# Kernel tuning notes

Hardware: AMD Instinct MI355X
Metric: run time of the kernel (lower is better)

The kernel has to match this reference:

```python
import jax, jax.numpy as jnp
import numpy as np

H = W = 128          # image shape
N_RGC = 32           # grid side -> 1024 RGCs per polarity
L = 1.0
K_POS = 0.155
V1_DIM = 64          # -> 4096 V1 units


def _build_model():
    rng = np.random.default_rng(0)
    pos = np.array([[i, j] for i in range(-N_RGC // 2, N_RGC // 2)
                    for j in range(-N_RGC // 2, N_RGC // 2)], dtype=np.float64)
    M = L * np.array([[1.0, 1.0], [np.sqrt(3.0), -np.sqrt(3.0)]])
    on_locs = pos @ M.T + rng.normal(0.0, K_POS * L, size=pos.shape)
    off_locs = pos @ M.T + rng.normal(0.0, K_POS * L, size=pos.shape)
    half = L * (N_RGC // 2)
    # clip (instead of filter) so RGC count is deterministic; boundary-only effect
    on_locs = np.clip(on_locs, -half, half)
    off_locs = np.clip(off_locs, -half, half)
    scale = H / (2.0 * half)
    on_locs = (on_locs + half) * scale
    off_locs = (off_locs + half) * scale
    locs = np.concatenate([on_locs, off_locs])          # [2048, 2]
    signs = np.concatenate([np.ones(len(on_locs)), -np.ones(len(off_locs))])
    sigma = 0.7 * L * scale

    # vectorized Gaussian RGC kernels: act[n, r, c] = exp(-((c-x_n)^2+(r-y_n)^2)/(2 sigma^2))
    gx = np.arange(H)[None, :] - locs[:, 0:1]           # [N, H] (column offsets)
    gy = np.arange(W)[None, :] - locs[:, 1:2]           # [N, W] (row offsets)
    acts = np.exp(-(gx[:, None, :] ** 2 + gy[:, :, None] ** 2) / (2.0 * sigma ** 2))
    acts = np.where(acts < 1e-5, 0.0, acts)
    acts /= acts.sum(axis=(1, 2), keepdims=True)
    acts *= signs[:, None, None]                        # [2048, 128, 128]

    n_rgc = locs.shape[0]
    lgn_idx = rng.integers(0, n_rgc, size=int(n_rgc * 1.5))  # [3072]
    lgn_locs = np.concatenate([locs, locs[lgn_idx]])         # [5120, 2]

    # V1 retinotopic grid
    X, Y = np.meshgrid(np.linspace(0, H, num=V1_DIM, endpoint=True),
                       np.linspace(0, W, num=V1_DIM, endpoint=True))
    v1_locs = np.vstack([X.ravel(), Y.ravel()]).T            # [4096, 2]

    # LGN->V1 connectivity (dense materialization of the CSR matrix)
    d2 = ((v1_locs[:, None, :] - lgn_locs[None, :, :]) ** 2).sum(-1)  # [4096, 5120]
    radius = 200.0 * sigma
    within = d2 <= radius ** 2
    p = (rng.random(d2.shape) >= 0.85 * np.exp(-d2 / (2.0 * sigma * 0.97))).astype(np.float64)
    conn = np.where(within, p * np.exp(-d2 / (2.0 * sigma * 1.1)), 0.0)

    return (acts[:n_rgc // 2].astype(np.float32),
            acts[n_rgc // 2:].astype(np.float32),
            conn.astype(np.float32),
            lgn_idx.astype(np.int32))


def setup_inputs() -> dict:
    key = jax.random.key(0)
    act_on, act_off, conn, lgn_idx = _build_model()
    x = jax.random.uniform(key, (H, W), dtype=jnp.float32)
    return {"x": x,
            "act_on": jnp.asarray(act_on),
            "act_off": jnp.asarray(act_off),
            "conn": jnp.asarray(conn),
            "lgn_idx": jnp.asarray(lgn_idx)}


def reference(x, act_on, act_off, conn, lgn_idx):
    # RGC stage: elementwise modulation of Gaussian kernels by image / inverted image
    n = act_on.shape[0] + act_off.shape[0]
    r = jnp.concatenate([x[None, :, :] * act_on,
                         (1.0 - x)[None, :, :] * act_off], axis=0).reshape(n, -1)  # [2048, 16384]
    # LGN stage: gather-based duplication
    l = jnp.concatenate([r, r[lgn_idx]], axis=0)                                    # [5120, 16384]
    # V1 stage: connectivity matmul (original: CSR SpMM)
    v = conn @ l                                                                    # [4096, 16384]
    return (r, l, v)
```

## Files before the change

kernel.cpp:

```cpp
#include <hip/hip_runtime.h>
#include <hip/hip_bf16.h>

#define NPIX   16384
#define NRROWS 2048
#define NLROWS 5120
#define NVROWS 4096
#define GK     5120
#define KF     2048
#define KEXTRA 3072
#define BK8    64
#define KTILES (KF / BK8)
#define NCB    (NPIX / 256)
#define TAU    1e-4f

using f32x4    = __attribute__((ext_vector_type(4))) float;
using bf16x8   = __attribute__((ext_vector_type(8))) __bf16;
using ushortx8 = __attribute__((ext_vector_type(8))) unsigned short;

__device__ __forceinline__ unsigned short f2b(float f) {
    union { float f; unsigned u; } v; v.f = f;
    unsigned r = (v.u + 0x7FFFu + ((v.u >> 16) & 1u)) >> 16;
    return (unsigned short)r;
}

#define GLOAD_LDS16(gsrc, ldst)                                                        \
    __builtin_amdgcn_global_load_lds(                                                  \
        (const __attribute__((address_space(1))) void*)(gsrc),                         \
        (__attribute__((address_space(3))) void*)(ldst), 16, 0, 0)

__global__ __launch_bounds__(256) void prep_kernel(const int* __restrict__ lgn_idx,
                                                   int* __restrict__ order,
                                                   int* __restrict__ inv_off,
                                                   int* __restrict__ inv_j,
                                                   unsigned int* __restrict__ amask) {
    __shared__ int bins[64];
    __shared__ int cnt[KF];
    __shared__ int part[256];
    __shared__ int spart[257];
    const int t = threadIdx.x;
    if (t < 64) bins[t] = 0;
    if (t < 16) amask[t] = 0u;
    __syncthreads();
    for (int k = t; k < KF; k += 256) {
        int base = k & 1023;
        int key = ((base >> 5) - (base & 31)) + 31;
        atomicAdd(&bins[key], 1);
    }
    __syncthreads();
    if (t == 0) {
        int run = 0;
        for (int b = 0; b < 63; ++b) { int c = bins[b]; bins[b] = run; run += c; }
    }
    __syncthreads();
    for (int k = t; k < KF; k += 256) {
        int base = k & 1023;
        int key = ((base >> 5) - (base & 31)) + 31;
        int slot = atomicAdd(&bins[key], 1);
        order[slot] = k;
    }
    for (int i = t; i < KF; i += 256) cnt[i] = 0;
    __syncthreads();
    for (int j = t; j < KEXTRA; j += 256) atomicAdd(&cnt[lgn_idx[j]], 1);
    __syncthreads();
    const int base8 = t * 8;
    int local[8];
    {
        int s = 0;
        #pragma unroll
        for (int i = 0; i < 8; ++i) { local[i] = s; s += cnt[base8 + i]; }
        part[t] = s;
    }
    __syncthreads();
    if (t == 0) {
        int run = 0;
        for (int i = 0; i < 256; ++i) { spart[i] = run; run += part[i]; }
        spart[256] = run;
    }
    __syncthreads();
    #pragma unroll
    for (int i = 0; i < 8; ++i) {
        int o = spart[t] + local[i];
        inv_off[base8 + i] = o;
        cnt[base8 + i] = o;
    }
    if (t == 0) inv_off[KF] = spart[256];
    __syncthreads();
    for (int j = t; j < KEXTRA; j += 256) {
        int s = atomicAdd(&cnt[lgn_idx[j]], 1);
        inv_j[s] = j;
    }
}

__global__ __launch_bounds__(256) void combo_kernel(const float* __restrict__ x,
                                                    const float* __restrict__ act_on,
                                                    const float* __restrict__ act_off,
                                                    const float* __restrict__ conn,
                                                    const int* __restrict__ lgn_idx,
                                                    const int* __restrict__ order,
                                                    const int* __restrict__ inv_off,
                                                    const int* __restrict__ inv_j,
                                                    float* __restrict__ r,
                                                    float* __restrict__ l,
                                                    unsigned short* __restrict__ rbt,
                                                    unsigned char* __restrict__ nzb,
                                                    unsigned short* __restrict__ Ab,
                                                    unsigned int* __restrict__ amask) {
    __shared__ unsigned short tile[64][66];
    __shared__ float acc[KF];
    __shared__ int nzf;
    __shared__ unsigned int rmask;
    const int t = threadIdx.x;

    if (blockIdx.y < KTILES) {
        const int k0 = blockIdx.y * 64;
        const int n0 = blockIdx.x * 64;
        if (t == 0) nzf = 0;
        __syncthreads();
        #pragma unroll
        for (int p = 0; p < 4; ++p) {
            int row  = p * 16 + (t >> 4);
            int kk   = k0 + row;
            int lrow = order[kk];
            int c4   = t & 15;
            int px   = n0 + c4 * 4;
            float4 xv = *reinterpret_cast<const float4*>(&x[px]);
            float4 d;
            if (lrow < 1024) {
                float4 a = *reinterpret_cast<const float4*>(&act_on[(size_t)lrow * NPIX + px]);
                d.x = xv.x * a.x; d.y = xv.y * a.y; d.z = xv.z * a.z; d.w = xv.w * a.w;
            } else {
                float4 a = *reinterpret_cast<const float4*>(&act_off[(size_t)(lrow - 1024) * NPIX + px]);
                d.x = (1.f - xv.x) * a.x; d.y = (1.f - xv.y) * a.y;
                d.z = (1.f - xv.z) * a.z; d.w = (1.f - xv.w) * a.w;
            }
            *reinterpret_cast<float4*>(&l[(size_t)lrow * NPIX + px]) = d;
            *reinterpret_cast<float4*>(&r[(size_t)lrow * NPIX + px]) = d;
            int e0 = inv_off[lrow], e1 = inv_off[lrow + 1];
            for (int e = e0; e < e1; ++e)
                *reinterpret_cast<float4*>(&l[(size_t)(NRROWS + inv_j[e]) * NPIX + px]) = d;
            tile[row][c4 * 4 + 0] = f2b(d.x);
            tile[row][c4 * 4 + 1] = f2b(d.y);
            tile[row][c4 * 4 + 2] = f2b(d.z);
            tile[row][c4 * 4 + 3] = f2b(d.w);
            if (d.x != 0.f || d.y != 0.f || d.z != 0.f || d.w != 0.f) nzf = 1;
        }
        __syncthreads();
        #pragma unroll
        for (int p = 0; p < 4; ++p) {
            int nn = p * 16 + (t >> 4);
            int k4 = t & 15;
            ushort4 s;
            s.x = tile[k4 * 4 + 0][nn];
            s.y = tile[k4 * 4 + 1][nn];
            s.z = tile[k4 * 4 + 2][nn];
            s.w = tile[k4 * 4 + 3][nn];
            *reinterpret_cast<ushort4*>(&rbt[(size_t)(n0 + nn) * KF + k0 + k4 * 4]) = s;
        }
        if (t == 0) nzb[blockIdx.y * 256 + blockIdx.x] = (unsigned char)nzf;
    } else {
        const int row = (blockIdx.y - KTILES) * 256 + blockIdx.x;
        if (t == 0) rmask = 0u;
        const float* crow = conn + (size_t)row * GK;
        #pragma unroll
        for (int i = 0; i < KF / 256; ++i)
            acc[t + 256 * i] = crow[t + 256 * i];
        __syncthreads();
        #pragma unroll
        for (int j = 0; j < KEXTRA / 256; ++j) {
            int jj = t + 256 * j;
            float v = crow[KF + jj];
            atomicAdd(&acc[lgn_idx[jj]], v);
        }
        __syncthreads();
        unsigned int local = 0u;
        #pragma unroll
        for (int i = 0; i < KF / 256; ++i) {
            int c = t + 256 * i;
            float v = acc[order[c]];
            Ab[(size_t)row * KF + c] = f2b(v);
            if (fabsf(v) >= TAU) local |= 1u << (c >> 6);
        }
        atomicOr(&rmask, local);
        __syncthreads();
        if (t == 0) atomicOr(&amask[row >> 8], rmask);
    }
}

__global__ __launch_bounds__(64) void bmask_build_kernel(const unsigned char* __restrict__ nzb,
                                                         unsigned int* __restrict__ bmask) {
    const int c = threadIdx.x;
    unsigned int m = 0u;
    for (int kt = 0; kt < KTILES; ++kt) {
        const unsigned char* p = nzb + kt * 256 + c * 4;
        if (p[0] | p[1] | p[2] | p[3]) m |= 1u << kt;
    }
    bmask[c] = m;
}

__global__ __launch_bounds__(512, 2) void gemm8_kernel(const unsigned short* __restrict__ Ab,
                                                       const unsigned short* __restrict__ Bb,
                                                       const unsigned int* __restrict__ bmask,
                                                       const unsigned int* __restrict__ amask,
                                                       float* __restrict__ C) {
    __shared__ unsigned short lds[2][2][256][64];
    __shared__ int s_klist[KTILES];
    __shared__ int s_cnt;

    const int tid  = threadIdx.x;
    const int lane = tid & 63;
    const int wid  = tid >> 6;
    const int wm   = wid >> 2;
    const int wn   = wid & 3;

    int bid = blockIdx.x;
    int swz = (bid & 7) * 128 + (bid >> 3);
    int mb  = swz & 15;
    int nb  = swz >> 4;
    const int row0 = mb * 256;
    const int col0 = nb * 256;

    if (tid == 0) {
        unsigned int m = bmask[nb] & amask[mb];
        int c = 0;
        while (m) { int kt = __ffs(m) - 1; m &= m - 1u; s_klist[c++] = kt; }
        s_cnt = c;
    }
    __syncthreads();
    const int cnt = s_cnt;

    const int strow = tid >> 3;
    const int gc    = (lane & 7) ^ (lane >> 3);

#define STAGE_A(buf, rnd, kt)                                                          \
    GLOAD_LDS16(&Ab[(size_t)(row0 + (rnd) * 64 + strow) * KF + (kt) * BK8 + gc * 8],   \
                &lds[buf][0][(rnd) * 64 + strow][(lane & 7) * 8])
#define STAGE_B(buf, rnd, kt)                                                          \
    GLOAD_LDS16(&Bb[(size_t)(col0 + (rnd) * 64 + strow) * KF + (kt) * BK8 + gc * 8],   \
                &lds[buf][1][(rnd) * 64 + strow][(lane & 7) * 8])
#define FRAG(buf, op, row, c)                                                          \
    __builtin_bit_cast(bf16x8, *reinterpret_cast<const ushortx8*>(                     \
        &lds[buf][op][row][(((c) ^ ((row) & 7)) * 8)]))

    f32x4 acc[2][2][4][2] = {};
    const int fr = lane & 15;
    const int kg = lane >> 4;

    bf16x8 af[2][4][2];
    bf16x8 b[2][2];

    if (cnt > 0) {
        const int kt0 = s_klist[0];
        STAGE_A(0, 0, kt0); STAGE_A(0, 1, kt0); STAGE_A(0, 2, kt0); STAGE_A(0, 3, kt0);
        STAGE_B(0, 0, kt0); STAGE_B(0, 1, kt0); STAGE_B(0, 2, kt0); STAGE_B(0, 3, kt0);
        asm volatile("s_waitcnt vmcnt(2)" ::: "memory");
        __builtin_amdgcn_s_barrier();

        for (int t = 0; t < cnt - 1; ++t) {
            const int cur = t & 1;
            const int nxt = cur ^ 1;
            const int ktn = s_klist[t + 1];

            #pragma unroll
            for (int m = 0; m < 4; ++m)
                #pragma unroll
                for (int ks = 0; ks < 2; ++ks)
                    af[0][m][ks] = FRAG(cur, 0, wm * 64 + m * 16 + fr, ks * 4 + kg);
            #pragma unroll
            for (int n = 0; n < 2; ++n)
                #pragma unroll
                for (int ks = 0; ks < 2; ++ks)
                    b[n][ks] = FRAG(cur, 1, wn * 32 + n * 16 + fr, ks * 4 + kg);
            STAGE_A(nxt, 0, ktn); STAGE_A(nxt, 1, ktn);
            STAGE_A(nxt, 2, ktn); STAGE_A(nxt, 3, ktn);
            __builtin_amdgcn_s_setprio(1);
            #pragma unroll
            for (int m = 0; m < 4; ++m)
                #pragma unroll
                for (int n = 0; n < 2; ++n)
                    #pragma unroll
                    for (int ks = 0; ks < 2; ++ks)
                        acc[0][0][m][n] = __builtin_amdgcn_mfma_f32_16x16x32_bf16(af[0][m][ks], b[n][ks], acc[0][0][m][n], 0, 0, 0);
            __builtin_amdgcn_s_setprio(0);

            #pragma unroll
            for (int m = 0; m < 4; ++m)
                #pragma unroll
                for (int ks = 0; ks < 2; ++ks)
                    af[1][m][ks] = FRAG(cur, 0, 128 + wm * 64 + m * 16 + fr, ks * 4 + kg);
            STAGE_B(nxt, 0, ktn); STAGE_B(nxt, 1, ktn);
            STAGE_B(nxt, 2, ktn); STAGE_B(nxt, 3, ktn);
            __builtin_amdgcn_s_setprio(1);
            #pragma unroll
            for (int m = 0; m < 4; ++m)
                #pragma unroll
                for (int n = 0; n < 2; ++n)
                    #pragma unroll
                    for (int ks = 0; ks < 2; ++ks)
                        acc[1][0][m][n] = __builtin_amdgcn_mfma_f32_16x16x32_bf16(af[1][m][ks], b[n][ks], acc[1][0][m][n], 0, 0, 0);
            __builtin_amdgcn_s_setprio(0);
            asm volatile("s_waitcnt vmcnt(8)" ::: "memory");
            __builtin_amdgcn_s_barrier();

            #pragma unroll
            for (int n = 0; n < 2; ++n)
                #pragma unroll
                for (int ks = 0; ks < 2; ++ks)
                    b[n][ks] = FRAG(cur, 1, 128 + wn * 32 + n * 16 + fr, ks * 4 + kg);
            __builtin_amdgcn_s_setprio(1);
            #pragma unroll
            for (int m = 0; m < 4; ++m)
                #pragma unroll
                for (int n = 0; n < 2; ++n)
                    #pragma unroll
                    for (int ks = 0; ks < 2; ++ks)
                        acc[1][1][m][n] = __builtin_amdgcn_mfma_f32_16x16x32_bf16(af[1][m][ks], b[n][ks], acc[1][1][m][n], 0, 0, 0);
            __builtin_amdgcn_s_setprio(0);

            __builtin_amdgcn_s_setprio(1);
            #pragma unroll
            for (int m = 0; m < 4; ++m)
                #pragma unroll
                for (int n = 0; n < 2; ++n)
                    #pragma unroll
                    for (int ks = 0; ks < 2; ++ks)
                        acc[0][1][m][n] = __builtin_amdgcn_mfma_f32_16x16x32_bf16(af[0][m][ks], b[n][ks], acc[0][1][m][n], 0, 0, 0);
            __builtin_amdgcn_s_setprio(0);
            asm volatile("s_waitcnt vmcnt(2)" ::: "memory");
            __builtin_amdgcn_s_barrier();
        }

        {
            const int cur = (cnt - 1) & 1;
            #pragma unroll
            for (int m = 0; m < 4; ++m)
                #pragma unroll
                for (int ks = 0; ks < 2; ++ks) {
                    af[0][m][ks] = FRAG(cur, 0, wm * 64 + m * 16 + fr, ks * 4 + kg);
                    af[1][m][ks] = FRAG(cur, 0, 128 + wm * 64 + m * 16 + fr, ks * 4 + kg);
                }
            #pragma unroll
            for (int n = 0; n < 2; ++n)
                #pragma unroll
                for (int ks = 0; ks < 2; ++ks)
                    b[n][ks] = FRAG(cur, 1, wn * 32 + n * 16 + fr, ks * 4 + kg);
            #pragma unroll
            for (int m = 0; m < 4; ++m)
                #pragma unroll
                for (int n = 0; n < 2; ++n)
                    #pragma unroll
                    for (int ks = 0; ks < 2; ++ks) {
                        acc[0][0][m][n] = __builtin_amdgcn_mfma_f32_16x16x32_bf16(af[0][m][ks], b[n][ks], acc[0][0][m][n], 0, 0, 0);
                        acc[1][0][m][n] = __builtin_amdgcn_mfma_f32_16x16x32_bf16(af[1][m][ks], b[n][ks], acc[1][0][m][n], 0, 0, 0);
                    }
            asm volatile("s_waitcnt vmcnt(0)" ::: "memory");
            __builtin_amdgcn_s_barrier();
            #pragma unroll
            for (int n = 0; n < 2; ++n)
                #pragma unroll
                for (int ks = 0; ks < 2; ++ks)
                    b[n][ks] = FRAG(cur, 1, 128 + wn * 32 + n * 16 + fr, ks * 4 + kg);
            #pragma unroll
            for (int m = 0; m < 4; ++m)
                #pragma unroll
                for (int n = 0; n < 2; ++n)
                    #pragma unroll
                    for (int ks = 0; ks < 2; ++ks) {
                        acc[1][1][m][n] = __builtin_amdgcn_mfma_f32_16x16x32_bf16(af[1][m][ks], b[n][ks], acc[1][1][m][n], 0, 0, 0);
                        acc[0][1][m][n] = __builtin_amdgcn_mfma_f32_16x16x32_bf16(af[0][m][ks], b[n][ks], acc[0][1][m][n], 0, 0, 0);
                    }
        }
    }

    #pragma unroll
    for (int qm = 0; qm < 2; ++qm)
        #pragma unroll
        for (int qn = 0; qn < 2; ++qn)
            #pragma unroll
            for (int m = 0; m < 4; ++m)
                #pragma unroll
                for (int n = 0; n < 2; ++n) {
                    int rr = row0 + qm * 128 + wm * 64 + m * 16 + kg * 4;
                    int cc = col0 + qn * 128 + wn * 32 + n * 16 + fr;
                    #pragma unroll
                    for (int j = 0; j < 4; ++j)
                        C[(size_t)(rr + j) * NPIX + cc] = acc[qm][qn][m][n][j];
                }
#undef STAGE_A
#undef STAGE_B
#undef FRAG
}

__global__ __launch_bounds__(256) void rgc_kernel(const float* __restrict__ x,
                                                  const float* __restrict__ act_on,
                                                  const float* __restrict__ act_off,
                                                  float* __restrict__ r) {
    unsigned f = blockIdx.x * 256u + threadIdx.x;
    unsigned n  = f >> 12;
    unsigned p4 = f & 4095u;
    float4 xv = reinterpret_cast<const float4*>(x)[p4];
    float4 a, o;
    if (n < 1024u) {
        a = reinterpret_cast<const float4*>(act_on)[(size_t)n * 4096u + p4];
        o.x = xv.x * a.x; o.y = xv.y * a.y; o.z = xv.z * a.z; o.w = xv.w * a.w;
    } else {
        a = reinterpret_cast<const float4*>(act_off)[(size_t)(n - 1024u) * 4096u + p4];
        o.x = (1.f - xv.x) * a.x; o.y = (1.f - xv.y) * a.y;
        o.z = (1.f - xv.z) * a.z; o.w = (1.f - xv.w) * a.w;
    }
    reinterpret_cast<float4*>(r)[f] = o;
}

__global__ __launch_bounds__(256) void lgn_kernel(const float* __restrict__ r,
                                                  const int* __restrict__ lgn_idx,
                                                  float* __restrict__ l) {
    unsigned f = blockIdx.x * 256u + threadIdx.x;
    unsigned k  = f >> 12;
    unsigned p4 = f & 4095u;
    unsigned src = (k < 2048u) ? k : (unsigned)lgn_idx[k - 2048u];
    reinterpret_cast<float4*>(l)[f] =
        reinterpret_cast<const float4*>(r)[(size_t)src * 4096u + p4];
}

__global__ __launch_bounds__(256) void gemm_fallback_kernel(const float* __restrict__ A,
                                                            const float* __restrict__ B,
                                                            float* __restrict__ C) {
    const int tid  = threadIdx.x;
    const int lane = tid & 63;
    const int wid  = tid >> 6;
    const int wr   = wid >> 1;
    const int wc   = wid & 1;
    const int row0 = blockIdx.y * 128;
    const int col0 = blockIdx.x * 128;

    __shared__ unsigned short As[4][128][8];
    __shared__ unsigned short Bs[4][128][8];

    f32x4 acc[4][4] = {};

    for (int k0 = 0; k0 < GK; k0 += 32) {
        #pragma unroll
        for (int i = 0; i < 4; ++i) {
            int f  = tid + 256 * i;
            int rr = f >> 3;
            int c4 = f & 7;
            float4 d = *reinterpret_cast<const float4*>(
                &A[(size_t)(row0 + rr) * GK + k0 + c4 * 4]);
            ushort4 s;
            s.x = f2b(d.x); s.y = f2b(d.y); s.z = f2b(d.z); s.w = f2b(d.w);
            *reinterpret_cast<ushort4*>(&As[c4 >> 1][rr][(c4 & 1) * 4]) = s;
        }
        #pragma unroll
        for (int i = 0; i < 4; ++i) {
            int f  = tid + 256 * i;
            int kk = f >> 5;
            int c4 = f & 31;
            float4 d = *reinterpret_cast<const float4*>(
                &B[(size_t)(k0 + kk) * NPIX + col0 + c4 * 4]);
            int g = kk >> 3, j = kk & 7;
            Bs[g][c4 * 4 + 0][j] = f2b(d.x);
            Bs[g][c4 * 4 + 1][j] = f2b(d.y);
            Bs[g][c4 * 4 + 2][j] = f2b(d.z);
            Bs[g][c4 * 4 + 3][j] = f2b(d.w);
        }
        __syncthreads();

        const int fr = lane & 15;
        const int kg = lane >> 4;
        bf16x8 af[4], bfr[4];
        #pragma unroll
        for (int m = 0; m < 4; ++m)
            af[m] = __builtin_bit_cast(bf16x8,
                *reinterpret_cast<const ushortx8*>(&As[kg][wr * 64 + m * 16 + fr][0]));
        #pragma unroll
        for (int n = 0; n < 4; ++n)
            bfr[n] = __builtin_bit_cast(bf16x8,
                *reinterpret_cast<const ushortx8*>(&Bs[kg][wc * 64 + n * 16 + fr][0]));
        #pragma unroll
        for (int m = 0; m < 4; ++m)
            #pragma unroll
            for (int n = 0; n < 4; ++n)
                acc[m][n] = __builtin_amdgcn_mfma_f32_16x16x32_bf16(af[m], bfr[n], acc[m][n], 0, 0, 0);
        __syncthreads();
    }

    #pragma unroll
    for (int m = 0; m < 4; ++m) {
        #pragma unroll
        for (int n = 0; n < 4; ++n) {
            int rr = row0 + wr * 64 + m * 16 + ((lane >> 4) << 2);
            int cc = col0 + wc * 64 + n * 16 + (lane & 15);
            #pragma unroll
            for (int j = 0; j < 4; ++j)
                C[(size_t)(rr + j) * NPIX + cc] = acc[m][n][j];
        }
    }
}

extern "C" void kernel_launch(void* const* d_in, const int* in_sizes, int n_in,
                              void* d_out, int out_size, void* d_ws, size_t ws_size,
                              hipStream_t stream) {
    const float* x       = (const float*)d_in[0];
    const float* act_on  = (const float*)d_in[1];
    const float* act_off = (const float*)d_in[2];
    const float* conn    = (const float*)d_in[3];
    const int*   lgn_idx = (const int*)d_in[4];

    float* out = (float*)d_out;
    float* r = out;
    float* l = out + (size_t)NRROWS * NPIX;
    float* v = out + (size_t)(NRROWS + NLROWS) * NPIX;

    const size_t rbt_bytes  = (size_t)NPIX * KF * sizeof(unsigned short);
    const size_t conn_bytes = (size_t)NVROWS * KF * sizeof(unsigned short);
    const size_t small_bytes = (KF + (KF + 1) + KEXTRA + NCB + 16 + 64) * sizeof(int)
                             + KTILES * 256;

    if (ws_size >= rbt_bytes + conn_bytes + small_bytes) {
        char* wsp = (char*)d_ws;
        unsigned short* rbt    = (unsigned short*)wsp;                wsp += rbt_bytes;
        unsigned short* connb  = (unsigned short*)wsp;                wsp += conn_bytes;
        int*            order  = (int*)wsp;                           wsp += KF * sizeof(int);
        int*            invoff = (int*)wsp;                           wsp += (KF + 1) * sizeof(int);
        int*            invj   = (int*)wsp;                           wsp += KEXTRA * sizeof(int);
        unsigned char*  nzb    = (unsigned char*)wsp;                 wsp += KTILES * 256;
        unsigned int*   bmask  = (unsigned int*)wsp;                  wsp += NCB * sizeof(int);
        unsigned int*   amask  = (unsigned int*)wsp;

        prep_kernel<<<1, 256, 0, stream>>>(lgn_idx, order, invoff, invj, amask);
        dim3 tg(NPIX / 64, KTILES + NVROWS / 256);
        combo_kernel<<<tg, 256, 0, stream>>>(x, act_on, act_off, conn, lgn_idx, order,
                                             invoff, invj, r, l, rbt, nzb, connb, amask);
        bmask_build_kernel<<<1, 64, 0, stream>>>(nzb, bmask);
        gemm8_kernel<<<(NVROWS / 256) * (NPIX / 256), 512, 0, stream>>>(connb, rbt, bmask, amask, v);
    } else {
        rgc_kernel<<<(NRROWS * (NPIX / 4)) / 256, 256, 0, stream>>>(x, act_on, act_off, r);
        lgn_kernel<<<(NLROWS * (NPIX / 4)) / 256, 256, 0, stream>>>(r, lgn_idx, l);
        dim3 grid(NPIX / 128, NVROWS / 128);
        gemm_fallback_kernel<<<grid, 256, 0, stream>>>(conn, l, v);
    }
}
```

Measured before the change: 313.2 us.

## Halve GEMM K-step to 32, raise occupancy, fold block-mask build into GEMM

Shrinks the LDS staging tile from 64 to 32 K elements, which halves shared memory per block and fragment registers, and raises launch bounds from 2 to 4 blocks per CU. The separate bmask_build kernel is removed: each GEMM block reads its nonzero flags from nzb directly and expands every active 64-wide tile into two 32-wide K steps. The aim is more latency hiding from higher occupancy and one fewer kernel launch. In exchange there are twice as many barriers and loop iterations per tile, and the LDS XOR swizzle is dropped, which may bring back bank conflicts.

After: 619.3 us. +97.7%, slower.

```diff
diff --git a/kernel.cpp b/kernel.cpp
--- a/kernel.cpp
+++ b/kernel.cpp
@@ -8,8 +8,7 @@
 #define GK     5120
 #define KF     2048
 #define KEXTRA 3072
-#define BK8    64
-#define KTILES (KF / BK8)
+#define KTILES 32
 #define NCB    (NPIX / 256)
 #define TAU    1e-4f
 
@@ -186,24 +185,14 @@
     }
 }
 
-__global__ __launch_bounds__(64) void bmask_build_kernel(const unsigned char* __restrict__ nzb,
-                                                         unsigned int* __restrict__ bmask) {
-    const int c = threadIdx.x;
-    unsigned int m = 0u;
-    for (int kt = 0; kt < KTILES; ++kt) {
-        const unsigned char* p = nzb + kt * 256 + c * 4;
-        if (p[0] | p[1] | p[2] | p[3]) m |= 1u << kt;
-    }
-    bmask[c] = m;
-}
-
-__global__ __launch_bounds__(512, 2) void gemm8_kernel(const unsigned short* __restrict__ Ab,
+__global__ __launch_bounds__(512, 4) void gemm8_kernel(const unsigned short* __restrict__ Ab,
                                                        const unsigned short* __restrict__ Bb,
-                                                       const unsigned int* __restrict__ bmask,
+                                                       const unsigned char* __restrict__ nzb,
                                                        const unsigned int* __restrict__ amask,
                                                        float* __restrict__ C) {
-    __shared__ unsigned short lds[2][2][256][64];
-    __shared__ int s_klist[KTILES];
+    __shared__ unsigned short lds[2][2][256][32];
+    __shared__ unsigned int s_ok[KTILES];
+    __shared__ int s_klist[2 * KTILES];
     __shared__ int s_cnt;
 
     const int tid  = threadIdx.x;
@@ -219,101 +208,89 @@
     const int row0 = mb * 256;
     const int col0 = nb * 256;
 
+    if (tid < KTILES)
+        s_ok[tid] = reinterpret_cast<const unsigned int*>(nzb)[tid * 64 + nb];
+    __syncthreads();
     if (tid == 0) {
-        unsigned int m = bmask[nb] & amask[mb];
+        unsigned int am = amask[mb];
         int c = 0;
-        while (m) { int kt = __ffs(m) - 1; m &= m - 1u; s_klist[c++] = kt; }
+        for (int kt = 0; kt < KTILES; ++kt)
+            if (s_ok[kt] && ((am >> kt) & 1u)) { s_klist[c++] = kt * 2; s_klist[c++] = kt * 2 + 1; }
         s_cnt = c;
     }
     __syncthreads();
     const int cnt = s_cnt;
 
-    const int strow = tid >> 3;
-    const int gc    = (lane & 7) ^ (lane >> 3);
-
-#define STAGE_A(buf, rnd, kt)                                                          \
-    GLOAD_LDS16(&Ab[(size_t)(row0 + (rnd) * 64 + strow) * KF + (kt) * BK8 + gc * 8],   \
-                &lds[buf][0][(rnd) * 64 + strow][(lane & 7) * 8])
-#define STAGE_B(buf, rnd, kt)                                                          \
-    GLOAD_LDS16(&Bb[(size_t)(col0 + (rnd) * 64 + strow) * KF + (kt) * BK8 + gc * 8],   \
-                &lds[buf][1][(rnd) * 64 + strow][(lane & 7) * 8])
-#define FRAG(buf, op, row, c)                                                          \
-    __builtin_bit_cast(bf16x8, *reinterpret_cast<const ushortx8*>(                     \
-        &lds[buf][op][row][(((c) ^ ((row) & 7)) * 8)]))
+    const int strow = tid >> 2;
+    const int kc    = lane & 3;
+
+#define STAGE_A(buf, half, ks)                                                          \
+    GLOAD_LDS16(&Ab[(size_t)(row0 + (half) * 128 + strow) * KF + (ks) * 32 + kc * 8],   \
+                &lds[buf][0][(half) * 128 + strow][kc * 8])
+#define STAGE_B(buf, half, ks)                                                          \
+    GLOAD_LDS16(&Bb[(size_t)(col0 + (half) * 128 + strow) * KF + (ks) * 32 + kc * 8],   \
+                &lds[buf][1][(half) * 128 + strow][kc * 8])
+#define FRAG(buf, op, row)                                                              \
+    __builtin_bit_cast(bf16x8, *reinterpret_cast<const ushortx8*>(                      \
+        &lds[buf][op][row][kg * 8]))
 
     f32x4 acc[2][2][4][2] = {};
     const int fr = lane & 15;
     const int kg = lane >> 4;
 
-    bf16x8 af[2][4][2];
-    bf16x8 b[2][2];
+    bf16x8 af[2][4];
+    bf16x8 b[2];
 
     if (cnt > 0) {
-        const int kt0 = s_klist[0];
-        STAGE_A(0, 0, kt0); STAGE_A(0, 1, kt0); STAGE_A(0, 2, kt0); STAGE_A(0, 3, kt0);
-        STAGE_B(0, 0, kt0); STAGE_B(0, 1, kt0); STAGE_B(0, 2, kt0); STAGE_B(0, 3, kt0);
-        asm volatile("s_waitcnt vmcnt(2)" ::: "memory");
+        const int ks0 = s_klist[0];
+        STAGE_A(0, 0, ks0); STAGE_A(0, 1, ks0);
+        STAGE_B(0, 0, ks0); STAGE_B(0, 1, ks0);
+        asm volatile("s_waitcnt vmcnt(1)" ::: "memory");
         __builtin_amdgcn_s_barrier();
 
         for (int t = 0; t < cnt - 1; ++t) {
             const int cur = t & 1;
             const int nxt = cur ^ 1;
-            const int ktn = s_klist[t + 1];
-
-            #pragma unroll
-            for (int m = 0; m < 4; ++m)
-                #pragma unroll
-                for (int ks = 0; ks < 2; ++ks)
-                    af[0][m][ks] = FRAG(cur, 0, wm * 64 + m * 16 + fr, ks * 4 + kg);
+            const int ksn = s_klist[t + 1];
+
+            #pragma unroll
+            for (int m = 0; m < 4; ++m)
+                af[0][m] = FRAG(cur, 0, wm * 64 + m * 16 + fr);
             #pragma unroll
             for (int n = 0; n < 2; ++n)
-                #pragma unroll
-                for (int ks = 0; ks < 2; ++ks)
-                    b[n][ks] = FRAG(cur, 1, wn * 32 + n * 16 + fr, ks * 4 + kg);
-            STAGE_A(nxt, 0, ktn); STAGE_A(nxt, 1, ktn);
-            STAGE_A(nxt, 2, ktn); STAGE_A(nxt, 3, ktn);
+                b[n] = FRAG(cur, 1, wn * 32 + n * 16 + fr);
+            STAGE_A(nxt, 0, ksn); STAGE_A(nxt, 1, ksn);
             __builtin_amdgcn_s_setprio(1);
             #pragma unroll
             for (int m = 0; m < 4; ++m)
                 #pragma unroll
                 for (int n = 0; n < 2; ++n)
-                    #pragma unroll
-                    for (int ks = 0; ks < 2; ++ks)
-                        acc[0][0][m][n] = __builtin_amdgcn_mfma_f32_16x16x32_bf16(af[0][m][ks], b[n][ks], acc[0][0][m][n], 0, 0, 0);
+                    acc[0][0][m][n] = __builtin_amdgcn_mfma_f32_16x16x32_bf16(af[0][m], b[n], acc[0][0][m][n], 0, 0, 0);
             __builtin_amdgcn_s_setprio(0);
 
             #pragma unroll
             for (int m = 0; m < 4; ++m)
-                #pragma unroll
-                for (int ks = 0; ks < 2; ++ks)
-                    af[1][m][ks] = FRAG(cur, 0, 128 + wm * 64 + m * 16 + fr, ks * 4 + kg);
-            STAGE_B(nxt, 0, ktn); STAGE_B(nxt, 1, ktn);
-            STAGE_B(nxt, 2, ktn); STAGE_B(nxt, 3, ktn);
+                af[1][m] = FRAG(cur, 0, 128 + wm * 64 + m * 16 + fr);
+            STAGE_B(nxt, 0, ksn); STAGE_B(nxt, 1, ksn);
             __builtin_amdgcn_s_setprio(1);
             #pragma unroll
             for (int m = 0; m < 4; ++m)
                 #pragma unroll
                 for (int n = 0; n < 2; ++n)
-                    #pragma unroll
-                    for (int ks = 0; ks < 2; ++ks)
-                        acc[1][0][m][n] = __builtin_amdgcn_mfma_f32_16x16x32_bf16(af[1][m][ks], b[n][ks], acc[1][0][m][n], 0, 0, 0);
+                    acc[1][0][m][n] = __builtin_amdgcn_mfma_f32_16x16x32_bf16(af[1][m], b[n], acc[1][0][m][n], 0, 0, 0);
             __builtin_amdgcn_s_setprio(0);
-            asm volatile("s_waitcnt vmcnt(8)" ::: "memory");
+            asm volatile("s_waitcnt vmcnt(4)" ::: "memory");
             __builtin_amdgcn_s_barrier();
 
             #pragma unroll
             for (int n = 0; n < 2; ++n)
-                #pragma unroll
-                for (int ks = 0; ks < 2; ++ks)
-                    b[n][ks] = FRAG(cur, 1, 128 + wn * 32 + n * 16 + fr, ks * 4 + kg);
+                b[n] = FRAG(cur, 1, 128 + wn * 32 + n * 16 + fr);
             __builtin_amdgcn_s_setprio(1);
             #pragma unroll
             for (int m = 0; m < 4; ++m)
                 #pragma unroll
                 for (int n = 0; n < 2; ++n)
-                    #pragma unroll
-                    for (int ks = 0; ks < 2; ++ks)
-                        acc[1][1][m][n] = __builtin_amdgcn_mfma_f32_16x16x32_bf16(af[1][m][ks], b[n][ks], acc[1][1][m][n], 0, 0, 0);
+                    acc[1][1][m][n] = __builtin_amdgcn_mfma_f32_16x16x32_bf16(af[1][m], b[n], acc[1][1][m][n], 0, 0, 0);
             __builtin_amdgcn_s_setprio(0);
 
             __builtin_amdgcn_s_setprio(1);
@@ -321,11 +298,9 @@
             for (int m = 0; m < 4; ++m)
                 #pragma unroll
                 for (int n = 0; n < 2; ++n)
-                    #pragma unroll
-                    for (int ks = 0; ks < 2; ++ks)
-                        acc[0][1][m][n] = __builtin_amdgcn_mfma_f32_16x16x32_bf16(af[0][m][ks], b[n][ks], acc[0][1][m][n], 0, 0, 0);
+                    acc[0][1][m][n] = __builtin_amdgcn_mfma_f32_16x16x32_bf16(af[0][m], b[n], acc[0][1][m][n], 0, 0, 0);
             __builtin_amdgcn_s_setprio(0);
-            asm volatile("s_waitcnt vmcnt(2)" ::: "memory");
+            asm volatile("s_waitcnt vmcnt(1)" ::: "memory");
             __builtin_amdgcn_s_barrier();
         }
 
@@ -333,41 +308,35 @@
             const int cur = (cnt - 1) & 1;
             #pragma unroll
             for (int m = 0; m < 4; ++m)
-                #pragma unroll
-                for (int ks = 0; ks < 2; ++ks) {
-                    af[0][m][ks] = FRAG(cur, 0, wm * 64 + m * 16 + fr, ks * 4 + kg);
-                    af[1][m][ks] = FRAG(cur, 0, 128 + wm * 64 + m * 16 + fr, ks * 4 + kg);
-                }
+                af[0][m] = FRAG(cur, 0, wm * 64 + m * 16 + fr);
             #pragma unroll
             for (int n = 0; n < 2; ++n)
-                #pragma unroll
-                for (int ks = 0; ks < 2; ++ks)
-                    b[n][ks] = FRAG(cur, 1, wn * 32 + n * 16 + fr, ks * 4 + kg);
+                b[n] = FRAG(cur, 1, wn * 32 + n * 16 + fr);
             #pragma unroll
             for (int m = 0; m < 4; ++m)
                 #pragma unroll
                 for (int n = 0; n < 2; ++n)
-                    #pragma unroll
-                    for (int ks = 0; ks < 2; ++ks) {
-                        acc[0][0][m][n] = __builtin_amdgcn_mfma_f32_16x16x32_bf16(af[0][m][ks], b[n][ks], acc[0][0][m][n], 0, 0, 0);
-                        acc[1][0][m][n] = __builtin_amdgcn_mfma_f32_16x16x32_bf16(af[1][m][ks], b[n][ks], acc[1][0][m][n], 0, 0, 0);
-                    }
+                    acc[0][0][m][n] = __builtin_amdgcn_mfma_f32_16x16x32_bf16(af[0][m], b[n], acc[0][0][m][n], 0, 0, 0);
+            #pragma unroll
+            for (int m = 0; m < 4; ++m)
+                af[1][m] = FRAG(cur, 0, 128 + wm * 64 + m * 16 + fr);
+            #pragma unroll
+            for (int m = 0; m < 4; ++m)
+                #pragma unroll
+                for (int n = 0; n < 2; ++n)
+                    acc[1][0][m][n] = __builtin_amdgcn_mfma_f32_16x16x32_bf16(af[1][m], b[n], acc[1][0][m][n], 0, 0, 0);
             asm volatile("s_waitcnt vmcnt(0)" ::: "memory");
             __builtin_amdgcn_s_barrier();
             #pragma unroll
             for (int n = 0; n < 2; ++n)
-                #pragma unroll
-                for (int ks = 0; ks < 2; ++ks)
-                    b[n][ks] = FRAG(cur, 1, 128 + wn * 32 + n * 16 + fr, ks * 4 + kg);
-            #pragma unroll
-            for (int m = 0; m < 4; ++m)
-                #pragma unroll
-                for (int n = 0; n < 2; ++n)
-                    #pragma unroll
-                    for (int ks = 0; ks < 2; ++ks) {
-                        acc[1][1][m][n] = __builtin_amdgcn_mfma_f32_16x16x32_bf16(af[1][m][ks], b[n][ks], acc[1][1][m][n], 0, 0, 0);
-                        acc[0][1][m][n] = __builtin_amdgcn_mfma_f32_16x16x32_bf16(af[0][m][ks], b[n][ks], acc[0][1][m][n], 0, 0, 0);
-                    }
+                b[n] = FRAG(cur, 1, 128 + wn * 32 + n * 16 + fr);
+            #pragma unroll
+            for (int m = 0; m < 4; ++m)
+                #pragma unroll
+                for (int n = 0; n < 2; ++n) {
+                    acc[1][1][m][n] = __builtin_amdgcn_mfma_f32_16x16x32_bf16(af[1][m], b[n], acc[1][1][m][n], 0, 0, 0);
+                    acc[0][1][m][n] = __builtin_amdgcn_mfma_f32_16x16x32_bf16(af[0][m], b[n], acc[0][1][m][n], 0, 0, 0);
+                }
         }
     }
 
@@ -512,7 +481,7 @@
 
     const size_t rbt_bytes  = (size_t)NPIX * KF * sizeof(unsigned short);
     const size_t conn_bytes = (size_t)NVROWS * KF * sizeof(unsigned short);
-    const size_t small_bytes = (KF + (KF + 1) + KEXTRA + NCB + 16 + 64) * sizeof(int)
+    const size_t small_bytes = (KF + (KF + 1) + KEXTRA + 16 + 64) * sizeof(int)
                              + KTILES * 256;
 
     if (ws_size >= rbt_bytes + conn_bytes + small_bytes) {
@@ -523,15 +492,13 @@
         int*            invoff = (int*)wsp;                           wsp += (KF + 1) * sizeof(int);
         int*            invj   = (int*)wsp;                           wsp += KEXTRA * sizeof(int);
         unsigned char*  nzb    = (unsigned char*)wsp;                 wsp += KTILES * 256;
-        unsigned int*   bmask  = (unsigned int*)wsp;                  wsp += NCB * sizeof(int);
         unsigned int*   amask  = (unsigned int*)wsp;
 
         prep_kernel<<<1, 256, 0, stream>>>(lgn_idx, order, invoff, invj, amask);
         dim3 tg(NPIX / 64, KTILES + NVROWS / 256);
         combo_kernel<<<tg, 256, 0, stream>>>(x, act_on, act_off, conn, lgn_idx, order,
                                              invoff, invj, r, l, rbt, nzb, connb, amask);
-        bmask_build_kernel<<<1, 64, 0, stream>>>(nzb, bmask);
-        gemm8_kernel<<<(NVROWS / 256) * (NPIX / 256), 512, 0, stream>>>(connb, rbt, bmask, amask, v);
+        gemm8_kernel<<<(NVROWS / 256) * (NPIX / 256), 512, 0, stream>>>(connb, rbt, nzb, amask, v);
     } else {
         rgc_kernel<<<(NRROWS * (NPIX / 4)) / 256, 256, 0, stream>>>(x, act_on, act_off, r);
         lgn_kernel<<<(NLROWS * (NPIX / 4)) / 256, 256, 0, stream>>>(r, lgn_idx, l);
```
